# Kernel tuning notes

Hardware: AMD Instinct MI355X
Metric: run time of the kernel (lower is better)

## Reference

```python
import jax, jax.numpy as jnp
import numpy as np

B, H, V = 4096, 2048, 32000
IGNORE_INDEX = -100
BETA = 0.1


def setup_inputs() -> dict:
    key = jax.random.key(0)
    kx, kw, ky = jax.random.split(key, 3)
    x = jax.random.normal(kx, (B, H), dtype=jnp.float32)
    # nn.Linear weight: shape (V, H), uniform(-1/sqrt(H), 1/sqrt(H))
    bound = 1.0 / np.sqrt(H)
    W = jax.random.uniform(kw, (V, H), dtype=jnp.float32, minval=-bound, maxval=bound)
    y = jax.random.randint(ky, (B,), 0, V, dtype=jnp.int64)
    return {"x": x, "W": W, "y": y}


def reference(x, W, y):
    # Linear projection: (B,H) @ (H,V) -> (B,V)
    logits = jnp.einsum("bh,vh->bv", x, W)
    half = logits.shape[0] // 2

    # Cross entropy (mean reduction, ignore_index) on the chosen half.
    logp = jax.nn.log_softmax(logits[:half], axis=-1)  # (half, V)
    y_half = y[:half]
    valid = y_half != IGNORE_INDEX
    safe_y = jnp.where(valid, y_half, 0)
    nll = -jnp.take_along_axis(logp, safe_y[:, None], axis=-1)[:, 0]
    nll = jnp.where(valid, nll, 0.0)
    ce_loss = nll.sum() / jnp.maximum(valid.sum(), 1).astype(nll.dtype)

    # Mean log-prob over the vocab dim for every row (as in the reference).
    all_logprobs = jax.nn.log_softmax(logits, axis=-1).mean(axis=-1)  # (B,)
    chosen = all_logprobs[:half]
    rejected = all_logprobs[half:]

    # ORPO odds-ratio loss
    log_odds = (chosen - rejected) - (
        jnp.log1p(-jnp.exp(chosen)) - jnp.log1p(-jnp.exp(rejected))
    )
    or_losses = BETA * jax.nn.log_sigmoid(log_odds)
    return ce_loss - or_losses.mean()
```

## Files before the change

### kernel.cpp

```cpp
#include <hip/hip_runtime.h>
#include <stdint.h>

#define BDIM 4096
#define HDIM 2048
#define VDIM 32000
#define HALF (BDIM / 2)
#define IGNORE_INDEX (-100)

typedef int   v8i  __attribute__((ext_vector_type(8)));
typedef int   v4i  __attribute__((ext_vector_type(4)));
typedef float v16f __attribute__((ext_vector_type(16)));
typedef float f32x4 __attribute__((ext_vector_type(4)));
typedef __bf16 bf16x8 __attribute__((ext_vector_type(8)));

#define AS1 __attribute__((address_space(1)))
#define AS3 __attribute__((address_space(3)))

__device__ __forceinline__ unsigned short f2bf(float f) {
    union { float f; unsigned int u; } v; v.f = f;
    unsigned int u = v.u;
    unsigned int r = u + 0x7FFFu + ((u >> 16) & 1u);
    return (unsigned short)(r >> 16);
}

__global__ void cvt_fp8_kernel(const float* __restrict__ x,
                               const float* __restrict__ W,
                               uint8_t* __restrict__ xq,
                               uint8_t* __restrict__ wq,
                               int nx4, int ntot4) {
    const int nth = gridDim.x * blockDim.x;
    const int t = blockIdx.x * blockDim.x + threadIdx.x;
    const int i0 = ((t >> 6) << 8) + (t & 63);
    const int stride = nth * 4;
    for (int i = i0; i < ntot4; i += stride) {
        const float4* s; unsigned* d; int j; float m;
        if (i < nx4) { s = (const float4*)x; d = (unsigned*)xq; j = i; m = 1.0f; }
        else         { s = (const float4*)W; d = (unsigned*)wq; j = i - nx4; m = 64.0f; }
        float4 f0 = s[j];
        float4 f1 = s[j + 64];
        float4 f2 = s[j + 128];
        float4 f3 = s[j + 192];
        int w;
        w = __builtin_amdgcn_cvt_pk_fp8_f32(f0.x * m, f0.y * m, 0, false);
        w = __builtin_amdgcn_cvt_pk_fp8_f32(f0.z * m, f0.w * m, w, true);
        d[j] = (unsigned)w;
        w = __builtin_amdgcn_cvt_pk_fp8_f32(f1.x * m, f1.y * m, 0, false);
        w = __builtin_amdgcn_cvt_pk_fp8_f32(f1.z * m, f1.w * m, w, true);
        d[j + 64] = (unsigned)w;
        w = __builtin_amdgcn_cvt_pk_fp8_f32(f2.x * m, f2.y * m, 0, false);
        w = __builtin_amdgcn_cvt_pk_fp8_f32(f2.z * m, f2.w * m, w, true);
        d[j + 128] = (unsigned)w;
        w = __builtin_amdgcn_cvt_pk_fp8_f32(f3.x * m, f3.y * m, 0, false);
        w = __builtin_amdgcn_cvt_pk_fp8_f32(f3.z * m, f3.w * m, w, true);
        d[j + 192] = (unsigned)w;
    }
}

__global__ __launch_bounds__(256, 4)
void gemm_reduce_fp8(const uint8_t* __restrict__ A, const uint8_t* __restrict__ B,
                     const int* __restrict__ y,
                     float* __restrict__ sumexp, float* __restrict__ sumlog,
                     float* __restrict__ tlog) {
    __shared__ uint8_t sA[2][128 * 64];
    __shared__ uint8_t sB[2][128 * 64];

    const int tid = threadIdx.x;
    const int lane = tid & 63;
    const int wave = tid >> 6;
    const int wm = wave >> 1, wn = wave & 1;
    const int m0 = blockIdx.x * 128;
    const int v0 = blockIdx.y * 128;

    v16f acc[2][2];
#pragma unroll
    for (int i = 0; i < 2; i++)
#pragma unroll
        for (int j = 0; j < 2; j++)
#pragma unroll
            for (int r = 0; r < 16; r++) acc[i][j][r] = 0.f;

    const int srow = wave * 32 + (lane >> 2);
    const int sc   = ((lane & 3) - ((lane >> 3) & 3)) & 3;
    const uint8_t* gA0 = A + (size_t)(m0 + srow) * HDIM + sc * 16;
    const uint8_t* gB0 = B + (size_t)(v0 + srow) * HDIM + sc * 16;
    const uint8_t* gA1 = gA0 + (size_t)16 * HDIM;
    const uint8_t* gB1 = gB0 + (size_t)16 * HDIM;
    const int lofs0 = (wave * 32) * 64;
    const int lofs1 = lofs0 + 16 * 64;

    const int fr32 = lane & 31;
    const int h = lane >> 5;
    const int swr = (fr32 >> 1) & 3;
    const int pos0 = (2 * h + swr) & 3;
    const int pos1 = (2 * h + 1 + swr) & 3;
    const int rA0 = (wm * 64 + fr32) * 64;
    const int rA1 = (wm * 64 + 32 + fr32) * 64;
    const int rB0 = (wn * 64 + fr32) * 64;
    const int rB1 = (wn * 64 + 32 + fr32) * 64;

#define STAGE(BUF, KT) do {                                                     \
        __builtin_amdgcn_global_load_lds(                                       \
            (const AS1 unsigned int*)(gA0 + (size_t)(KT) * 64),                 \
            (AS3 unsigned int*)(&sA[BUF][lofs0]), 16, 0, 0);                    \
        __builtin_amdgcn_global_load_lds(                                       \
            (const AS1 unsigned int*)(gA1 + (size_t)(KT) * 64),                 \
            (AS3 unsigned int*)(&sA[BUF][lofs1]), 16, 0, 0);                    \
        __builtin_amdgcn_global_load_lds(                                       \
            (const AS1 unsigned int*)(gB0 + (size_t)(KT) * 64),                 \
            (AS3 unsigned int*)(&sB[BUF][lofs0]), 16, 0, 0);                    \
        __builtin_amdgcn_global_load_lds(                                       \
            (const AS1 unsigned int*)(gB1 + (size_t)(KT) * 64),                 \
            (AS3 unsigned int*)(&sB[BUF][lofs1]), 16, 0, 0);                    \
    } while (0)

#define KSTEP(BUF, VMASM) do {                                                  \
        asm volatile(VMASM ::: "memory");                                       \
        __builtin_amdgcn_sched_barrier(0);                                      \
        __builtin_amdgcn_s_barrier();                                           \
        const v4i* pA0 = (const v4i*)&sA[BUF][rA0];                             \
        const v4i* pA1 = (const v4i*)&sA[BUF][rA1];                             \
        const v4i* pB0 = (const v4i*)&sB[BUF][rB0];                             \
        const v4i* pB1 = (const v4i*)&sB[BUF][rB1];                             \
        v4i a00 = pA0[pos0], a01 = pA0[pos1];                                   \
        v4i a10 = pA1[pos0], a11 = pA1[pos1];                                   \
        v4i b00 = pB0[pos0], b01 = pB0[pos1];                                   \
        v4i b10 = pB1[pos0], b11 = pB1[pos1];                                   \
        v8i af0 = {a00[0], a00[1], a00[2], a00[3], a01[0], a01[1], a01[2], a01[3]}; \
        v8i af1 = {a10[0], a10[1], a10[2], a10[3], a11[0], a11[1], a11[2], a11[3]}; \
        v8i bf0 = {b00[0], b00[1], b00[2], b00[3], b01[0], b01[1], b01[2], b01[3]}; \
        v8i bf1 = {b10[0], b10[1], b10[2], b10[3], b11[0], b11[1], b11[2], b11[3]}; \
        __builtin_amdgcn_s_setprio(1);                                          \
        acc[0][0] = __builtin_amdgcn_mfma_scale_f32_32x32x64_f8f6f4(            \
            af0, bf0, acc[0][0], 0, 0, 0, 0x7F7F7F7F, 0, 0x7F7F7F7F);           \
        acc[0][1] = __builtin_amdgcn_mfma_scale_f32_32x32x64_f8f6f4(            \
            af0, bf1, acc[0][1], 0, 0, 0, 0x7F7F7F7F, 0, 0x7F7F7F7F);           \
        acc[1][0] = __builtin_amdgcn_mfma_scale_f32_32x32x64_f8f6f4(            \
            af1, bf0, acc[1][0], 0, 0, 0, 0x7F7F7F7F, 0, 0x7F7F7F7F);           \
        acc[1][1] = __builtin_amdgcn_mfma_scale_f32_32x32x64_f8f6f4(            \
            af1, bf1, acc[1][1], 0, 0, 0, 0x7F7F7F7F, 0, 0x7F7F7F7F);           \
        __builtin_amdgcn_s_setprio(0);                                          \
        __builtin_amdgcn_s_barrier();                                           \
    } while (0)

    STAGE(0, 0);
    for (int kt = 0; kt < 30; kt += 2) {
        STAGE(1, kt + 1);
        KSTEP(0, "s_waitcnt vmcnt(4)");
        STAGE(0, kt + 2);
        KSTEP(1, "s_waitcnt vmcnt(4)");
    }
    STAGE(1, 31);
    KSTEP(0, "s_waitcnt vmcnt(4)");
    KSTEP(1, "s_waitcnt vmcnt(0)");

#undef STAGE
#undef KSTEP

    const float s64 = 0.015625f;
#pragma unroll
    for (int mi = 0; mi < 2; mi++) {
        const int baseRow = m0 + wm * 64 + mi * 32;
#pragma unroll
        for (int reg = 0; reg < 16; reg++) {
            float va = acc[mi][0][reg] * s64;
            float vb = acc[mi][1][reg] * s64;
            float e = __expf(va) + __expf(vb);
            float sm = va + vb;
#pragma unroll
            for (int off = 1; off < 32; off <<= 1) {
                e  += __shfl_xor(e, off);
                sm += __shfl_xor(sm, off);
            }
            int row = baseRow + (reg & 3) + 8 * (reg >> 2) + 4 * h;
            if (fr32 == 0) {
                atomicAdd(&sumexp[row], e);
                atomicAdd(&sumlog[row], sm);
            }
            int yv = y[row];
            int c0 = v0 + wn * 64 + fr32;
            if (c0 == yv) tlog[row] = va;
            if (c0 + 32 == yv) tlog[row] = vb;
        }
    }
}

__global__ __launch_bounds__(256, 4)
void gemm_reduce_f32(const float* __restrict__ A, const float* __restrict__ B,
                     const int* __restrict__ y,
                     float* __restrict__ sumexp, float* __restrict__ sumlog,
                     float* __restrict__ tlog) {
    __shared__ unsigned short sA[128 * 32];
    __shared__ unsigned short sB[128 * 32];

    const int tid  = threadIdx.x;
    const int lane = tid & 63;
    const int wave = tid >> 6;
    const int wm = wave >> 1, wn = wave & 1;
    const int m0 = blockIdx.x * 128;
    const int v0 = blockIdx.y * 128;
    const int fr = lane & 15;
    const int fq = lane >> 4;
    const int swz = (fr >> 1) & 3;

    f32x4 acc[4][4];
#pragma unroll
    for (int i = 0; i < 4; i++)
#pragma unroll
        for (int j = 0; j < 4; j++) acc[i][j] = (f32x4){0.f, 0.f, 0.f, 0.f};

    const int r8 = tid >> 3;
    const int kc = (tid & 7) * 4;
    for (int kt = 0; kt < HDIM; kt += 32) {
#pragma unroll
        for (int p = 0; p < 4; p++) {
            int row = p * 32 + r8;
            int pos = ((kc >> 3) ^ ((row >> 1) & 3)) * 8 + (kc & 7);
            float4 fa = *(const float4*)&A[(size_t)(m0 + row) * HDIM + kt + kc];
            float4 fb = *(const float4*)&B[(size_t)(v0 + row) * HDIM + kt + kc];
            ushort4 ua, ub;
            ua.x = f2bf(fa.x); ua.y = f2bf(fa.y); ua.z = f2bf(fa.z); ua.w = f2bf(fa.w);
            ub.x = f2bf(fb.x); ub.y = f2bf(fb.y); ub.z = f2bf(fb.z); ub.w = f2bf(fb.w);
            *(ushort4*)&sA[row * 32 + pos] = ua;
            *(ushort4*)&sB[row * 32 + pos] = ub;
        }
        __syncthreads();

        bf16x8 af[4], bf[4];
#pragma unroll
        for (int i = 0; i < 4; i++) {
            af[i] = *(const bf16x8*)&sA[(wm * 64 + i * 16 + fr) * 32 + (fq ^ swz) * 8];
            bf[i] = *(const bf16x8*)&sB[(wn * 64 + i * 16 + fr) * 32 + (fq ^ swz) * 8];
        }
#pragma unroll
        for (int mi = 0; mi < 4; mi++)
#pragma unroll
            for (int ni = 0; ni < 4; ni++)
                acc[mi][ni] = __builtin_amdgcn_mfma_f32_16x16x32_bf16(
                    af[mi], bf[ni], acc[mi][ni], 0, 0, 0);
        __syncthreads();
    }

    const int baseRow = m0 + wm * 64;
    const int cbase = v0 + wn * 64 + fr;
#pragma unroll
    for (int mi = 0; mi < 4; mi++) {
        float se[4] = {0.f, 0.f, 0.f, 0.f};
        float sl[4] = {0.f, 0.f, 0.f, 0.f};
#pragma unroll
        for (int ni = 0; ni < 4; ni++)
#pragma unroll
            for (int r = 0; r < 4; r++) {
                float v = acc[mi][ni][r];
                se[r] += __expf(v);
                sl[r] += v;
            }
#pragma unroll
        for (int r = 0; r < 4; r++) {
            float e = se[r], s = sl[r];
#pragma unroll
            for (int off = 1; off < 16; off <<= 1) {
                e += __shfl_xor(e, off);
                s += __shfl_xor(s, off);
            }
            int row = baseRow + mi * 16 + fq * 4 + r;
            if (fr == 0) {
                atomicAdd(&sumexp[row], e);
                atomicAdd(&sumlog[row], s);
            }
            int yv = y[row];
#pragma unroll
            for (int ni = 0; ni < 4; ni++)
                if (cbase + ni * 16 == yv) tlog[row] = acc[mi][ni][r];
        }
    }
}

__global__ void finalize_kernel(const float* __restrict__ sumexp,
                                const float* __restrict__ sumlog,
                                const float* __restrict__ tlog,
                                const int* __restrict__ y,
                                float* __restrict__ out) {
    __shared__ float red[3][4];
    float s_nll = 0.f, s_or = 0.f, cnt = 0.f;
    for (int p = threadIdx.x; p < HALF; p += blockDim.x) {
        float lse_c = logf(sumexp[p]);
        float lse_r = logf(sumexp[p + HALF]);
        float mc = sumlog[p] * (1.0f / VDIM);
        float mr = sumlog[p + HALF] * (1.0f / VDIM);
        int yv = y[p];
        if (yv != IGNORE_INDEX) { s_nll += lse_c - tlog[p]; cnt += 1.f; }
        float ch = mc - lse_c, rj = mr - lse_r;
        float lo = (ch - rj) - (log1pf(-expf(ch)) - log1pf(-expf(rj)));
        float ls = fminf(lo, 0.f) - log1pf(expf(-fabsf(lo)));
        s_or += 0.1f * ls;
    }
    for (int off = 32; off; off >>= 1) {
        s_nll += __shfl_down(s_nll, off);
        s_or  += __shfl_down(s_or, off);
        cnt   += __shfl_down(cnt, off);
    }
    int wave = threadIdx.x >> 6, lane = threadIdx.x & 63;
    if (lane == 0) { red[0][wave] = s_nll; red[1][wave] = s_or; red[2][wave] = cnt; }
    __syncthreads();
    if (threadIdx.x == 0) {
        float tn = 0.f, to = 0.f, tc = 0.f;
        for (int w = 0; w < 4; w++) { tn += red[0][w]; to += red[1][w]; tc += red[2][w]; }
        out[0] = tn / fmaxf(tc, 1.f) - to / (float)HALF;
    }
}

extern "C" void kernel_launch(void* const* d_in, const int* in_sizes, int n_in,
                              void* d_out, int out_size, void* d_ws, size_t ws_size,
                              hipStream_t stream) {
    const float* x = (const float*)d_in[0];
    const float* W = (const float*)d_in[1];
    const int* y   = (const int*)d_in[2];
    float* out     = (float*)d_out;

    float* sumexp = (float*)d_ws;
    float* sumlog = sumexp + BDIM;
    float* tlog   = sumlog + BDIM;
    hipMemsetAsync(d_ws, 0, 3 * BDIM * sizeof(float), stream);

    const size_t bfoff = 65536;
    const size_t xcount = (size_t)BDIM * HDIM;
    const size_t wcount = (size_t)VDIM * HDIM;
    const size_t need = bfoff + xcount + wcount;

    dim3 grid(BDIM / 128, VDIM / 128);
    if (ws_size >= need) {
        uint8_t* xq = (uint8_t*)d_ws + bfoff;
        uint8_t* wq = xq + xcount;
        int nx4 = (int)(xcount / 4);
        int ntot4 = (int)((xcount + wcount) / 4);
        cvt_fp8_kernel<<<4096, 256, 0, stream>>>(x, W, xq, wq, nx4, ntot4);
        gemm_reduce_fp8<<<grid, 256, 0, stream>>>(xq, wq, y, sumexp, sumlog, tlog);
    } else {
        gemm_reduce_f32<<<grid, 256, 0, stream>>>(x, W, y, sumexp, sumlog, tlog);
    }
    finalize_kernel<<<1, 256, 0, stream>>>(sumexp, sumlog, tlog, y, out);
}
```

Before: 868.9 us.

## Split fp8 conversion into per-tensor kernels and simplify GEMM k-loop sync

Replaces the grid-stride fused conversion kernel with separate one-shot kernels for x and W, and replaces the hand-tuned vmcnt waits, sched barriers and setprio in the GEMM k-loop with plain __syncthreads. The W conversion kernel is launched twice, which duplicates a full read of W and write of wq. The simpler sync drops the explicit partial vmcnt wait and may change how global loads overlap with MFMA work.

```diff
diff --git a/kernel.cpp b/kernel.cpp
--- a/kernel.cpp
+++ b/kernel.cpp
@@ -23,37 +23,41 @@
     return (unsigned short)(r >> 16);
 }
 
-__global__ void cvt_fp8_kernel(const float* __restrict__ x,
-                               const float* __restrict__ W,
-                               uint8_t* __restrict__ xq,
-                               uint8_t* __restrict__ wq,
-                               int nx4, int ntot4) {
-    const int nth = gridDim.x * blockDim.x;
-    const int t = blockIdx.x * blockDim.x + threadIdx.x;
-    const int i0 = ((t >> 6) << 8) + (t & 63);
-    const int stride = nth * 4;
-    for (int i = i0; i < ntot4; i += stride) {
-        const float4* s; unsigned* d; int j; float m;
-        if (i < nx4) { s = (const float4*)x; d = (unsigned*)xq; j = i; m = 1.0f; }
-        else         { s = (const float4*)W; d = (unsigned*)wq; j = i - nx4; m = 64.0f; }
-        float4 f0 = s[j];
-        float4 f1 = s[j + 64];
-        float4 f2 = s[j + 128];
-        float4 f3 = s[j + 192];
-        int w;
-        w = __builtin_amdgcn_cvt_pk_fp8_f32(f0.x * m, f0.y * m, 0, false);
-        w = __builtin_amdgcn_cvt_pk_fp8_f32(f0.z * m, f0.w * m, w, true);
-        d[j] = (unsigned)w;
-        w = __builtin_amdgcn_cvt_pk_fp8_f32(f1.x * m, f1.y * m, 0, false);
-        w = __builtin_amdgcn_cvt_pk_fp8_f32(f1.z * m, f1.w * m, w, true);
-        d[j + 64] = (unsigned)w;
-        w = __builtin_amdgcn_cvt_pk_fp8_f32(f2.x * m, f2.y * m, 0, false);
-        w = __builtin_amdgcn_cvt_pk_fp8_f32(f2.z * m, f2.w * m, w, true);
-        d[j + 128] = (unsigned)w;
-        w = __builtin_amdgcn_cvt_pk_fp8_f32(f3.x * m, f3.y * m, 0, false);
-        w = __builtin_amdgcn_cvt_pk_fp8_f32(f3.z * m, f3.w * m, w, true);
-        d[j + 192] = (unsigned)w;
-    }
+
+__device__ __forceinline__ void cvt4_store(const float4* __restrict__ s,
+                                           unsigned* __restrict__ d,
+                                           int j, float m) {
+    float4 f0 = s[j];
+    float4 f1 = s[j + 64];
+    float4 f2 = s[j + 128];
+    float4 f3 = s[j + 192];
+    int w;
+    w = __builtin_amdgcn_cvt_pk_fp8_f32(f0.x * m, f0.y * m, 0, false);
+    w = __builtin_amdgcn_cvt_pk_fp8_f32(f0.z * m, f0.w * m, w, true);
+    d[j] = (unsigned)w;
+    w = __builtin_amdgcn_cvt_pk_fp8_f32(f1.x * m, f1.y * m, 0, false);
+    w = __builtin_amdgcn_cvt_pk_fp8_f32(f1.z * m, f1.w * m, w, true);
+    d[j + 64] = (unsigned)w;
+    w = __builtin_amdgcn_cvt_pk_fp8_f32(f2.x * m, f2.y * m, 0, false);
+    w = __builtin_amdgcn_cvt_pk_fp8_f32(f2.z * m, f2.w * m, w, true);
+    d[j + 128] = (unsigned)w;
+    w = __builtin_amdgcn_cvt_pk_fp8_f32(f3.x * m, f3.y * m, 0, false);
+    w = __builtin_amdgcn_cvt_pk_fp8_f32(f3.z * m, f3.w * m, w, true);
+    d[j + 192] = (unsigned)w;
+}
+
+__global__ __launch_bounds__(256) void cvt_x_kernel(const float* __restrict__ x,
+                                                    uint8_t* __restrict__ xq) {
+    const int t = blockIdx.x * 256 + threadIdx.x;
+    const int j = ((t >> 6) << 8) + (t & 63);
+    cvt4_store((const float4*)x, (unsigned*)xq, j, 1.0f);
+}
+
+__global__ __launch_bounds__(256) void cvt_w_kernel(const float* __restrict__ W,
+                                                    uint8_t* __restrict__ wq) {
+    const int t = blockIdx.x * 256 + threadIdx.x;
+    const int j = ((t >> 6) << 8) + (t & 63);
+    cvt4_store((const float4*)W, (unsigned*)wq, j, 64.0f);
 }
 
 __global__ __launch_bounds__(256, 4)
@@ -98,25 +102,22 @@
     const int rB0 = (wn * 64 + fr32) * 64;
     const int rB1 = (wn * 64 + 32 + fr32) * 64;
 
-#define STAGE(BUF, KT) do {                                                     \
+#define STAGE(BUF, SL) do {                                                     \
         __builtin_amdgcn_global_load_lds(                                       \
-            (const AS1 unsigned int*)(gA0 + (size_t)(KT) * 64),                 \
+            (const AS1 unsigned int*)(gA0 + (size_t)(SL) * 64),                 \
             (AS3 unsigned int*)(&sA[BUF][lofs0]), 16, 0, 0);                    \
         __builtin_amdgcn_global_load_lds(                                       \
-            (const AS1 unsigned int*)(gA1 + (size_t)(KT) * 64),                 \
+            (const AS1 unsigned int*)(gA1 + (size_t)(SL) * 64),                 \
             (AS3 unsigned int*)(&sA[BUF][lofs1]), 16, 0, 0);                    \
         __builtin_amdgcn_global_load_lds(                                       \
-            (const AS1 unsigned int*)(gB0 + (size_t)(KT) * 64),                 \
+            (const AS1 unsigned int*)(gB0 + (size_t)(SL) * 64),                 \
             (AS3 unsigned int*)(&sB[BUF][lofs0]), 16, 0, 0);                    \
         __builtin_amdgcn_global_load_lds(                                       \
-            (const AS1 unsigned int*)(gB1 + (size_t)(KT) * 64),                 \
+            (const AS1 unsigned int*)(gB1 + (size_t)(SL) * 64),                 \
             (AS3 unsigned int*)(&sB[BUF][lofs1]), 16, 0, 0);                    \
     } while (0)
 
-#define KSTEP(BUF, VMASM) do {                                                  \
-        asm volatile(VMASM ::: "memory");                                       \
-        __builtin_amdgcn_sched_barrier(0);                                      \
-        __builtin_amdgcn_s_barrier();                                           \
+#define COMPUTE(BUF) do {                                                       \
         const v4i* pA0 = (const v4i*)&sA[BUF][rA0];                             \
         const v4i* pA1 = (const v4i*)&sA[BUF][rA1];                             \
         const v4i* pB0 = (const v4i*)&sB[BUF][rB0];                             \
@@ -129,7 +130,6 @@
         v8i af1 = {a10[0], a10[1], a10[2], a10[3], a11[0], a11[1], a11[2], a11[3]}; \
         v8i bf0 = {b00[0], b00[1], b00[2], b00[3], b01[0], b01[1], b01[2], b01[3]}; \
         v8i bf1 = {b10[0], b10[1], b10[2], b10[3], b11[0], b11[1], b11[2], b11[3]}; \
-        __builtin_amdgcn_s_setprio(1);                                          \
         acc[0][0] = __builtin_amdgcn_mfma_scale_f32_32x32x64_f8f6f4(            \
             af0, bf0, acc[0][0], 0, 0, 0, 0x7F7F7F7F, 0, 0x7F7F7F7F);           \
         acc[0][1] = __builtin_amdgcn_mfma_scale_f32_32x32x64_f8f6f4(            \
@@ -138,23 +138,25 @@
             af1, bf0, acc[1][0], 0, 0, 0, 0x7F7F7F7F, 0, 0x7F7F7F7F);           \
         acc[1][1] = __builtin_amdgcn_mfma_scale_f32_32x32x64_f8f6f4(            \
             af1, bf1, acc[1][1], 0, 0, 0, 0x7F7F7F7F, 0, 0x7F7F7F7F);           \
-        __builtin_amdgcn_s_setprio(0);                                          \
-        __builtin_amdgcn_s_barrier();                                           \
     } while (0)
 
     STAGE(0, 0);
-    for (int kt = 0; kt < 30; kt += 2) {
-        STAGE(1, kt + 1);
-        KSTEP(0, "s_waitcnt vmcnt(4)");
-        STAGE(0, kt + 2);
-        KSTEP(1, "s_waitcnt vmcnt(4)");
+    __syncthreads();
+    for (int i = 0; i < 30; i += 2) {
+        STAGE(1, i + 1);
+        COMPUTE(0);
+        __syncthreads();
+        STAGE(0, i + 2);
+        COMPUTE(1);
+        __syncthreads();
     }
     STAGE(1, 31);
-    KSTEP(0, "s_waitcnt vmcnt(4)");
-    KSTEP(1, "s_waitcnt vmcnt(0)");
+    COMPUTE(0);
+    __syncthreads();
+    COMPUTE(1);
 
 #undef STAGE
-#undef KSTEP
+#undef COMPUTE
 
     const float s64 = 0.015625f;
 #pragma unroll
@@ -327,15 +329,16 @@
     const size_t wcount = (size_t)VDIM * HDIM;
     const size_t need = bfoff + xcount + wcount;
 
-    dim3 grid(BDIM / 128, VDIM / 128);
     if (ws_size >= need) {
         uint8_t* xq = (uint8_t*)d_ws + bfoff;
         uint8_t* wq = xq + xcount;
-        int nx4 = (int)(xcount / 4);
-        int ntot4 = (int)((xcount + wcount) / 4);
-        cvt_fp8_kernel<<<4096, 256, 0, stream>>>(x, W, xq, wq, nx4, ntot4);
+        cvt_x_kernel<<<2048, 256, 0, stream>>>(x, xq);
+        cvt_w_kernel<<<16000, 256, 0, stream>>>(W, wq);
+        cvt_w_kernel<<<16000, 256, 0, stream>>>(W, wq);
+        dim3 grid(BDIM / 128, VDIM / 128);
         gemm_reduce_fp8<<<grid, 256, 0, stream>>>(xq, wq, y, sumexp, sumlog, tlog);
     } else {
+        dim3 grid(BDIM / 128, VDIM / 128);
         gemm_reduce_f32<<<grid, 256, 0, stream>>>(x, W, y, sumexp, sumlog, tlog);
     }
     finalize_kernel<<<1, 256, 0, stream>>>(sumexp, sumlog, tlog, y, out);
```

Measured after the change: 977.0 us. 12.4% more time.
